# Kernel optimization log

Measured on AMD Instinct MI355X. Metric: run time of the kernel, lower is better.

The kernel has to match this reference:

```python
import jax, jax.numpy as jnp
import numpy as np

TEMPERATURE = 0.07
LOSS_CL_WEIGHT = 1.0
EPS = 1e-12  # F.normalize default eps


def setup_inputs() -> dict:
    key = jax.random.key(0)
    k1, k2 = jax.random.split(key)
    N, S, D = 64, 64, 256
    return {
        "proj_z1": jax.random.normal(k1, (N, S, D), dtype=jnp.float32),
        "proj_z2": jax.random.normal(k2, (N, S, D), dtype=jnp.float32),
    }


def _clean_normalize(x, NS, D):
    # flatten -> replace nan/inf with 0 -> L2 normalize rows
    x = x.reshape(NS, D)
    x = jnp.where(jnp.isfinite(x), x, jnp.zeros((), x.dtype))
    norm = jnp.linalg.norm(x, axis=1, keepdims=True)
    return x / jnp.maximum(norm, EPS)


def reference(proj_z1, proj_z2):
    N, S, D = proj_z1.shape
    NS = N * S
    M = 2 * NS
    f1 = _clean_normalize(proj_z1, NS, D)
    f2 = _clean_normalize(proj_z2, NS, D)
    features = jnp.concatenate([f1, f2], axis=0)          # (M, D)
    sim = features @ features.T                            # (M, M)

    idx = jnp.arange(M)
    # positive pair: row i <-> row (i + NS) mod M (eye blocks in label_matrix)
    positives = sim[idx, (idx + NS) % M] / TEMPERATURE     # (M,)
    # CE denominator = all off-diagonal entries (positives + negatives)
    scores = sim / TEMPERATURE
    scores = jnp.where(idx[:, None] == idx[None, :], -jnp.inf, scores)
    lse = jax.nn.logsumexp(scores, axis=1)                 # (M,)
    loss = jnp.mean(lse - positives)
    return LOSS_CL_WEIGHT * loss
```

## Files before the change

kernel.cpp:

```cpp
#include <hip/hip_runtime.h>
#include <hip/hip_bf16.h>

#define NS_ 4096
#define M_  8192
#define D_  256
#define TEMP 0.07f
#define EXP_SCALE (1.4426950408889634f / 0.07f)
#define LN2 0.6931471805599453f

typedef short bf16x8 __attribute__((ext_vector_type(8)));
typedef float f32x4  __attribute__((ext_vector_type(4)));
typedef unsigned short ushortx4 __attribute__((ext_vector_type(4)));

static __device__ inline unsigned short f2bf(float x) {
    unsigned u = __float_as_uint(x);
    u += 0x7fffu + ((u >> 16) & 1u);
    return (unsigned short)(u >> 16);
}

static __device__ inline float cleanf(float v) {
    return __builtin_isfinite(v) ? v : 0.0f;
}

__global__ __launch_bounds__(64) void knorm(const float* __restrict__ z1,
                                            const float* __restrict__ z2,
                                            short* __restrict__ F,
                                            float* __restrict__ pos) {
    const int i = blockIdx.x;
    const int t = threadIdx.x;
    const float4* p1 = (const float4*)(z1 + (size_t)i * D_);
    const float4* p2 = (const float4*)(z2 + (size_t)i * D_);
    float4 a = p1[t], b = p2[t];
    a.x = cleanf(a.x); a.y = cleanf(a.y); a.z = cleanf(a.z); a.w = cleanf(a.w);
    b.x = cleanf(b.x); b.y = cleanf(b.y); b.z = cleanf(b.z); b.w = cleanf(b.w);

    float s1 = a.x*a.x + a.y*a.y + a.z*a.z + a.w*a.w;
    float s2 = b.x*b.x + b.y*b.y + b.z*b.z + b.w*b.w;
    float dp = a.x*b.x + a.y*b.y + a.z*b.z + a.w*b.w;
    #pragma unroll
    for (int m = 1; m < 64; m <<= 1) {
        s1 += __shfl_xor(s1, m);
        s2 += __shfl_xor(s2, m);
        dp += __shfl_xor(dp, m);
    }
    const float inv1 = 1.0f / fmaxf(sqrtf(s1), 1e-12f);
    const float inv2 = 1.0f / fmaxf(sqrtf(s2), 1e-12f);

    ushortx4 o1, o2;
    o1.x = f2bf(a.x * inv1); o1.y = f2bf(a.y * inv1); o1.z = f2bf(a.z * inv1); o1.w = f2bf(a.w * inv1);
    o2.x = f2bf(b.x * inv2); o2.y = f2bf(b.y * inv2); o2.z = f2bf(b.z * inv2); o2.w = f2bf(b.w * inv2);
    ((ushortx4*)(F + (size_t)i * D_))[t]          = o1;
    ((ushortx4*)(F + (size_t)(i + NS_) * D_))[t]  = o2;

    if (t == 0) pos[i] = dp * inv1 * inv2;
}

#define BLDS_STRIDE 264
__global__ __launch_bounds__(256) void kgemm(const short* __restrict__ F,
                                             float* __restrict__ denom) {
    __shared__ short Bl[64 * BLDS_STRIDE];

    const int rtile = blockIdx.x >> 2;
    const int cq    = blockIdx.x & 3;
    const int R0 = rtile * 64;
    const int C0 = cq * 2048;

    const int tid  = threadIdx.x;
    const int lane = tid & 63;
    const int wave = tid >> 6;
    const int c16  = lane & 15;
    const int quad = lane >> 4;

    bf16x8 afrag[8];
    {
        const short* ap = F + (size_t)(R0 + wave * 16 + c16) * D_ + quad * 8;
        #pragma unroll
        for (int ks = 0; ks < 8; ++ks)
            afrag[ks] = *(const bf16x8*)(ap + ks * 32);
    }

    float accexp[4] = {0.f, 0.f, 0.f, 0.f};
    const int grow0 = R0 + wave * 16 + quad * 4;

    for (int it = 0; it < 32; ++it) {
        __syncthreads();
        {
            const uint4* src = (const uint4*)(F + (size_t)(C0 + it * 64) * D_);
            #pragma unroll
            for (int r2 = 0; r2 < 8; ++r2) {
                int c   = tid + r2 * 256;
                int row = c >> 5;
                int k   = c & 31;
                *(uint4*)(&Bl[row * BLDS_STRIDE + k * 8]) = src[row * 32 + k];
            }
        }
        __syncthreads();

        #pragma unroll
        for (int sub = 0; sub < 4; ++sub) {
            const short* bp = &Bl[(sub * 16 + c16) * BLDS_STRIDE + quad * 8];
            f32x4 acc = {0.f, 0.f, 0.f, 0.f};
            #pragma unroll
            for (int ks = 0; ks < 8; ++ks) {
                bf16x8 bfrag = *(const bf16x8*)(bp + ks * 32);
                acc = __builtin_amdgcn_mfma_f32_16x16x32_bf16(afrag[ks], bfrag, acc, 0, 0, 0);
            }
            const int gcol = C0 + it * 64 + sub * 16 + c16;
            #pragma unroll
            for (int r = 0; r < 4; ++r) {
                float e = __builtin_amdgcn_exp2f(acc[r] * EXP_SCALE);
                if (grow0 + r == gcol) e = 0.0f;
                accexp[r] += e;
            }
        }
    }

    #pragma unroll
    for (int r = 0; r < 4; ++r) {
        float v = accexp[r];
        v += __shfl_xor(v, 1);
        v += __shfl_xor(v, 2);
        v += __shfl_xor(v, 4);
        v += __shfl_xor(v, 8);
        if (c16 == 0) atomicAdd(&denom[grow0 + r], v);
    }
}

__global__ __launch_bounds__(256) void kfinal(const float* __restrict__ denom,
                                              const float* __restrict__ pos,
                                              float* __restrict__ out) {
    const int tid = threadIdx.x;
    float sl = 0.f, sp = 0.f;
    for (int i = tid; i < M_; i += 256)
        sl += __builtin_amdgcn_logf(denom[i]) * LN2;
    for (int i = tid; i < NS_; i += 256)
        sp += pos[i];
    #pragma unroll
    for (int m = 1; m < 64; m <<= 1) {
        sl += __shfl_xor(sl, m);
        sp += __shfl_xor(sp, m);
    }
    __shared__ float redL[4], redP[4];
    const int wave = tid >> 6, lane = tid & 63;
    if (lane == 0) { redL[wave] = sl; redP[wave] = sp; }
    __syncthreads();
    if (tid == 0) {
        float SL = redL[0] + redL[1] + redL[2] + redL[3];
        float SP = redP[0] + redP[1] + redP[2] + redP[3];
        out[0] = (SL - 2.0f * SP / TEMP) / (float)M_;
    }
}

extern "C" void kernel_launch(void* const* d_in, const int* in_sizes, int n_in,
                              void* d_out, int out_size, void* d_ws, size_t ws_size,
                              hipStream_t stream) {
    const float* z1 = (const float*)d_in[0];
    const float* z2 = (const float*)d_in[1];

    short* F     = (short*)d_ws;
    float* denom = (float*)((char*)d_ws + (size_t)M_ * D_ * 2);
    float* pos   = denom + M_;
    float* out   = (float*)d_out;

    hipMemsetAsync(denom, 0, M_ * sizeof(float), stream);
    knorm<<<NS_, 64, 0, stream>>>(z1, z2, F, pos);
    kgemm<<<512, 256, 0, stream>>>(F, denom);
    kfinal<<<1, 256, 0, stream>>>(denom, pos, out);
}
```

Baseline: 132.6 us.

## Restructure similarity GEMM with 4x A reuse, direct LDS loads, fused final reduction

Each wave now holds A fragments for all four 16-row subtiles and computes one 16-column slice against all of them. Each B fragment read from LDS therefore feeds four MFMAs instead of one. B tiles are staged through global_load_lds with an XOR-swizzled layout instead of a padded stride, and the per-element diagonal test now runs only on diagonal subtiles. The final kernel is removed: positives go straight to the output through atomics in knorm, and the last block per row tile computes the log terms using a counter. The cost is more registers (launch bounds allow 2 blocks) and many atomics on a single output scalar.

```diff
diff --git a/kernel.cpp b/kernel.cpp
--- a/kernel.cpp
+++ b/kernel.cpp
@@ -1,11 +1,12 @@
 #include <hip/hip_runtime.h>
 #include <hip/hip_bf16.h>
+#include <stdint.h>
 
 #define NS_ 4096
 #define M_  8192
 #define D_  256
 #define TEMP 0.07f
-#define EXP_SCALE (1.4426950408889634f / 0.07f)
+#define EXP_SCALE 20.61707212818536f
 #define LN2 0.6931471805599453f
 
 typedef short bf16x8 __attribute__((ext_vector_type(8)));
@@ -22,10 +23,14 @@
     return __builtin_isfinite(v) ? v : 0.0f;
 }
 
+#define LDS_LOAD16(gp, lp) \
+    __builtin_amdgcn_global_load_lds((const __attribute__((address_space(1))) uint32_t*)(gp), \
+                                     (__attribute__((address_space(3))) uint32_t*)(lp), 16, 0, 0)
+
 __global__ __launch_bounds__(64) void knorm(const float* __restrict__ z1,
                                             const float* __restrict__ z2,
                                             short* __restrict__ F,
-                                            float* __restrict__ pos) {
+                                            float* __restrict__ out) {
     const int i = blockIdx.x;
     const int t = threadIdx.x;
     const float4* p1 = (const float4*)(z1 + (size_t)i * D_);
@@ -52,13 +57,15 @@
     ((ushortx4*)(F + (size_t)i * D_))[t]          = o1;
     ((ushortx4*)(F + (size_t)(i + NS_) * D_))[t]  = o2;
 
-    if (t == 0) pos[i] = dp * inv1 * inv2;
+    if (t == 0) atomicAdd(out, dp * inv1 * inv2 * (-2.0f / (TEMP * (float)M_)));
 }
 
-#define BLDS_STRIDE 264
-__global__ __launch_bounds__(256) void kgemm(const short* __restrict__ F,
-                                             float* __restrict__ denom) {
-    __shared__ short Bl[64 * BLDS_STRIDE];
+__global__ __launch_bounds__(256, 2) void kgemm(const short* __restrict__ F,
+                                                float* __restrict__ denom,
+                                                int* __restrict__ cnt,
+                                                float* __restrict__ out) {
+    __shared__ short Bl[64 * 256];
+    __shared__ int lastflag;
 
     const int rtile = blockIdx.x >> 2;
     const int cq    = blockIdx.x & 3;
@@ -71,83 +78,100 @@
     const int c16  = lane & 15;
     const int quad = lane >> 4;
 
-    bf16x8 afrag[8];
-    {
-        const short* ap = F + (size_t)(R0 + wave * 16 + c16) * D_ + quad * 8;
+    bf16x8 afrag[4][8];
+    #pragma unroll
+    for (int s = 0; s < 4; ++s) {
+        const short* ap = F + (size_t)(R0 + s * 16 + c16) * D_ + quad * 8;
         #pragma unroll
         for (int ks = 0; ks < 8; ++ks)
-            afrag[ks] = *(const bf16x8*)(ap + ks * 32);
+            afrag[s][ks] = *(const bf16x8*)(ap + ks * 32);
     }
 
-    float accexp[4] = {0.f, 0.f, 0.f, 0.f};
-    const int grow0 = R0 + wave * 16 + quad * 4;
+    int goff[8];
+    #pragma unroll
+    for (int r2 = 0; r2 < 8; ++r2) {
+        int c    = tid + r2 * 256;
+        int trow = c >> 5;
+        int kg   = (c & 31) ^ (trow & 7);
+        goff[r2] = trow * D_ + kg * 8;
+    }
+    const int tc = wave * 16 + c16;
+    int boff[8];
+    #pragma unroll
+    for (int ks = 0; ks < 8; ++ks)
+        boff[ks] = tc * 256 + (((ks * 4 + quad) ^ (tc & 7)) * 8);
+
+    float accexp[4][4];
+    #pragma unroll
+    for (int s = 0; s < 4; ++s)
+        #pragma unroll
+        for (int r = 0; r < 4; ++r) accexp[s][r] = 0.0f;
 
     for (int it = 0; it < 32; ++it) {
         __syncthreads();
-        {
-            const uint4* src = (const uint4*)(F + (size_t)(C0 + it * 64) * D_);
-            #pragma unroll
-            for (int r2 = 0; r2 < 8; ++r2) {
-                int c   = tid + r2 * 256;
-                int row = c >> 5;
-                int k   = c & 31;
-                *(uint4*)(&Bl[row * BLDS_STRIDE + k * 8]) = src[row * 32 + k];
-            }
-        }
+        const short* gb = F + (size_t)(C0 + it * 64) * D_;
+        #pragma unroll
+        for (int r2 = 0; r2 < 8; ++r2)
+            LDS_LOAD16(gb + goff[r2], Bl + (tid + r2 * 256) * 8);
         __syncthreads();
 
+        bf16x8 bfrag[8];
         #pragma unroll
-        for (int sub = 0; sub < 4; ++sub) {
-            const short* bp = &Bl[(sub * 16 + c16) * BLDS_STRIDE + quad * 8];
-            f32x4 acc = {0.f, 0.f, 0.f, 0.f};
+        for (int ks = 0; ks < 8; ++ks)
+            bfrag[ks] = *(const bf16x8*)(Bl + boff[ks]);
+
+        f32x4 acc[4];
+        #pragma unroll
+        for (int s = 0; s < 4; ++s) acc[s] = (f32x4){0.f, 0.f, 0.f, 0.f};
+        #pragma unroll
+        for (int ks = 0; ks < 8; ++ks)
             #pragma unroll
-            for (int ks = 0; ks < 8; ++ks) {
-                bf16x8 bfrag = *(const bf16x8*)(bp + ks * 32);
-                acc = __builtin_amdgcn_mfma_f32_16x16x32_bf16(afrag[ks], bfrag, acc, 0, 0, 0);
-            }
-            const int gcol = C0 + it * 64 + sub * 16 + c16;
-            #pragma unroll
-            for (int r = 0; r < 4; ++r) {
-                float e = __builtin_amdgcn_exp2f(acc[r] * EXP_SCALE);
-                if (grow0 + r == gcol) e = 0.0f;
-                accexp[r] += e;
+            for (int s = 0; s < 4; ++s)
+                acc[s] = __builtin_amdgcn_mfma_f32_16x16x32_bf16(afrag[s][ks], bfrag[ks], acc[s], 0, 0, 0);
+
+        const int colbase = C0 + it * 64 + wave * 16;
+        #pragma unroll
+        for (int s = 0; s < 4; ++s) {
+            if (colbase != R0 + s * 16) {
+                #pragma unroll
+                for (int r = 0; r < 4; ++r)
+                    accexp[s][r] += __builtin_amdgcn_exp2f(acc[s][r] * EXP_SCALE);
+            } else {
+                #pragma unroll
+                for (int r = 0; r < 4; ++r) {
+                    float e = __builtin_amdgcn_exp2f(acc[s][r] * EXP_SCALE);
+                    if (c16 == quad * 4 + r) e = 0.0f;
+                    accexp[s][r] += e;
+                }
             }
         }
     }
 
     #pragma unroll
-    for (int r = 0; r < 4; ++r) {
-        float v = accexp[r];
-        v += __shfl_xor(v, 1);
-        v += __shfl_xor(v, 2);
-        v += __shfl_xor(v, 4);
-        v += __shfl_xor(v, 8);
-        if (c16 == 0) atomicAdd(&denom[grow0 + r], v);
-    }
-}
+    for (int s = 0; s < 4; ++s)
+        #pragma unroll
+        for (int r = 0; r < 4; ++r) {
+            float v = accexp[s][r];
+            v += __shfl_xor(v, 1);
+            v += __shfl_xor(v, 2);
+            v += __shfl_xor(v, 4);
+            v += __shfl_xor(v, 8);
+            if (c16 == 0) atomicAdd(&denom[R0 + s * 16 + quad * 4 + r], v);
+        }
 
-__global__ __launch_bounds__(256) void kfinal(const float* __restrict__ denom,
-                                              const float* __restrict__ pos,
-                                              float* __restrict__ out) {
-    const int tid = threadIdx.x;
-    float sl = 0.f, sp = 0.f;
-    for (int i = tid; i < M_; i += 256)
-        sl += __builtin_amdgcn_logf(denom[i]) * LN2;
-    for (int i = tid; i < NS_; i += 256)
-        sp += pos[i];
-    #pragma unroll
-    for (int m = 1; m < 64; m <<= 1) {
-        sl += __shfl_xor(sl, m);
-        sp += __shfl_xor(sp, m);
-    }
-    __shared__ float redL[4], redP[4];
-    const int wave = tid >> 6, lane = tid & 63;
-    if (lane == 0) { redL[wave] = sl; redP[wave] = sp; }
     __syncthreads();
     if (tid == 0) {
-        float SL = redL[0] + redL[1] + redL[2] + redL[3];
-        float SP = redP[0] + redP[1] + redP[2] + redP[3];
-        out[0] = (SL - 2.0f * SP / TEMP) / (float)M_;
+        __threadfence();
+        lastflag = (atomicAdd(&cnt[rtile], 1) == 3);
+    }
+    __syncthreads();
+    if (lastflag && tid < 64) {
+        __threadfence();
+        float v = atomicAdd(&denom[R0 + tid], 0.0f);
+        float p = __builtin_amdgcn_logf(v) * (LN2 / (float)M_);
+        #pragma unroll
+        for (int m = 1; m < 64; m <<= 1) p += __shfl_xor(p, m);
+        if (tid == 0) atomicAdd(out, p);
     }
 }
 
@@ -159,11 +183,11 @@
 
     short* F     = (short*)d_ws;
     float* denom = (float*)((char*)d_ws + (size_t)M_ * D_ * 2);
-    float* pos   = denom + M_;
+    int*   cnt   = (int*)(denom + M_);
     float* out   = (float*)d_out;
 
-    hipMemsetAsync(denom, 0, M_ * sizeof(float), stream);
-    knorm<<<NS_, 64, 0, stream>>>(z1, z2, F, pos);
-    kgemm<<<512, 256, 0, stream>>>(F, denom);
-    kfinal<<<1, 256, 0, stream>>>(denom, pos, out);
+    hipMemsetAsync(denom, 0, M_ * sizeof(float) + 128 * sizeof(int), stream);
+    hipMemsetAsync(out, 0, sizeof(float), stream);
+    knorm<<<NS_, 64, 0, stream>>>(z1, z2, F, out);
+    kgemm<<<512, 256, 0, stream>>>(F, denom, cnt, out);
 }
```

Result: slower. 174.6 us (+31.7%).
